# Kernel tuning notes

Measured on AMD Instinct MI355X. Metric: run time of the kernel, lower is better.

The kernel has to match this reference:

```python
import jax, jax.numpy as jnp
import numpy as np

NUM_HEADS = 16
ROPE_BASE = 10000.0


def _rotate_half(x):
    x1 = x[..., ::2]
    x2 = x[..., 1::2]
    return jnp.stack((-x2, x1), axis=-1).reshape(x.shape)


def _rope_tables(seq_len, head_dim, dtype):
    inv_freq = 1.0 / (ROPE_BASE ** (jnp.arange(0, head_dim, 2, dtype=jnp.float32) / head_dim))
    t = jnp.arange(seq_len, dtype=jnp.float32)
    freqs = jnp.outer(t, inv_freq)            # [S, head_dim//2]
    emb = jnp.concatenate((freqs, freqs), -1)  # [S, head_dim]
    return jnp.cos(emb).astype(dtype), jnp.sin(emb).astype(dtype)


def setup_inputs() -> dict:
    key = jax.random.key(0)
    ks = jax.random.split(key, 5)
    B, S, H = 1, 4096, 1024
    scale = 1.0 / np.sqrt(H)
    return {
        "x": jax.random.normal(ks[0], (B, S, H), jnp.float32),
        "Wq": jax.random.normal(ks[1], (H, H), jnp.float32) * scale,
        "Wk": jax.random.normal(ks[2], (H, H), jnp.float32) * scale,
        "Wv": jax.random.normal(ks[3], (H, H), jnp.float32) * scale,
        "Wo": jax.random.normal(ks[4], (H, H), jnp.float32) * scale,
        "attention_mask": jnp.ones((B, S), jnp.int32),
    }


def reference(x, Wq, Wk, Wv, Wo, attention_mask):
    B, S, H = x.shape
    hd = H // NUM_HEADS

    def split_heads(t):  # [B,S,H] -> [B,nh,S,hd]
        return t.reshape(B, S, NUM_HEADS, hd).transpose(0, 2, 1, 3)

    q = split_heads(x @ Wq)
    k = split_heads(x @ Wk)
    v = split_heads(x @ Wv)

    cos, sin = _rope_tables(S, hd, x.dtype)
    cos = cos[None, None]  # [1,1,S,hd]
    sin = sin[None, None]
    q = q * cos + _rotate_half(q) * sin
    k = k * cos + _rotate_half(k) * sin

    scores = jnp.einsum("bhqd,bhkd->bhqk", q, k) / jnp.sqrt(jnp.asarray(hd, x.dtype))
    mask = attention_mask.reshape(B, 1, 1, S)
    scores = jnp.where(mask == 0, jnp.finfo(x.dtype).min, scores)
    probs = jax.nn.softmax(scores, axis=-1)
    ctx = jnp.einsum("bhqk,bhkd->bhqd", probs, v)
    ctx = ctx.transpose(0, 2, 1, 3).reshape(B, S, H)
    return ctx @ Wo
```

## Files before the change

kernel.cpp:

```cpp
#include <hip/hip_runtime.h>
#include <cstdint>
#include <cstddef>

#define S_LEN 4096
#define NHEADS 16
#define HD 64
#define HDIM 1024

typedef _Float16 f16x8 __attribute__((ext_vector_type(8)));
typedef __fp16 h16x2 __attribute__((ext_vector_type(2)));
typedef float f32x4 __attribute__((ext_vector_type(4)));
typedef unsigned char uchar;
typedef unsigned int u32;

__device__ __forceinline__ f32x4 mfma16h(f16x8 a, f16x8 b, f32x4 c) {
    return __builtin_amdgcn_mfma_f32_16x16x32_f16(a, b, c, 0, 0, 0);
}
__device__ __forceinline__ void async16(void* lds, const void* g) {
    __builtin_amdgcn_global_load_lds(
        (const __attribute__((address_space(1))) u32*)g,
        (__attribute__((address_space(3))) u32*)lds, 16, 0, 0);
}


__global__ __launch_bounds__(256) void pack_xw(
    const float* __restrict__ X, uchar* __restrict__ P,
    const int* __restrict__ M, _Float16* __restrict__ FM16,
    const float* __restrict__ W0, const float* __restrict__ W1,
    const float* __restrict__ W2, const float* __restrict__ W3,
    uchar* __restrict__ PW)
{
    if (blockIdx.x < 2048) {
        int id = blockIdx.x * 256 + threadIdx.x;
        int m = id >> 7, g = id & 127;
        int kc = g >> 3, b = g & 7;
        float v[8];
        *(float4*)&v[0] = *(const float4*)&X[(size_t)m * HDIM + kc * 64 + b * 8];
        *(float4*)&v[4] = *(const float4*)&X[(size_t)m * HDIM + kc * 64 + b * 8 + 4];
        __align__(16) _Float16 h[8];
        #pragma unroll
        for (int i = 0; i < 8; i++) h[i] = (_Float16)v[i];
        size_t base = ((size_t)(m * 16 + kc)) * 128 + (size_t)((b ^ (m & 7)) * 16);
        *(uint4*)(P + base) = *(const uint4*)h;
        if (id < S_LEN) {
            int c = id >> 7, k128 = id & 127;
            int w = k128 >> 5, k32 = k128 & 31;
            int q = (k32 >> 2) & 3, kt = k32 >> 4, r = k32 & 3;
            FM16[c * 128 + w * 32 + q * 8 + kt * 4 + r] =
                (_Float16)((M[id] == 0) ? 0.0f : 1.0f);
        }
    } else {
        int id = (blockIdx.x - 2048) * 256 + threadIdx.x;
        int wsel = id >> 17;
        int lid  = id & 131071;
        int g = lid >> 10, n = lid & 1023;
        int kc = g >> 3, b = g & 7;
        const float* W = (wsel == 0) ? W0 : (wsel == 1) ? W1 : (wsel == 2) ? W2 : W3;
        uchar* dst = PW + (size_t)wsel * 2097152;
        float v[8];
        #pragma unroll
        for (int j = 0; j < 8; j++)
            v[j] = W[(size_t)(kc * 64 + b * 8 + j) * HDIM + n];
        __align__(16) _Float16 h[8];
        #pragma unroll
        for (int i = 0; i < 8; i++) h[i] = (_Float16)v[i];
        size_t base = ((size_t)(n * 16 + kc)) * 128 + (size_t)((b ^ (n & 7)) * 16);
        *(uint4*)(dst + base) = *(const uint4*)h;
    }
}

__global__ __launch_bounds__(256) void gemm_qkv(
    const uchar* __restrict__ Ap, const uchar* __restrict__ Bp,
    const int* __restrict__ M,
    uchar* __restrict__ Qg, uchar* __restrict__ Kg, uchar* __restrict__ Vg)
{
    __shared__ __align__(16) uchar AB[65536];
    const int t = threadIdx.x, lane = t & 63, w = t >> 6;
    const int quad = lane >> 4, l15 = lane & 15, x7 = l15 & 7;
    const int m0 = blockIdx.y * 128, n0 = blockIdx.x * 128;
    const int wm = (w >> 1) * 64, wn = (w & 1) * 64;

    f32x4 acc[4][4];
    const f32x4 zero4 = {0.0f, 0.0f, 0.0f, 0.0f};
    #pragma unroll
    for (int mt = 0; mt < 4; mt++)
        #pragma unroll
        for (int nt = 0; nt < 4; nt++) acc[mt][nt] = zero4;

    #pragma unroll
    for (int i = 0; i < 4; i++) {
        int idx = i * 256 + t;
        int row = idx >> 3, blk = idx & 7;
        int ldso = (idx & ~63) * 16;
        async16(AB + ldso,         Ap + ((size_t)((m0 + row) * 16 + 0)) * 128 + blk * 16);
        async16(AB + 16384 + ldso, Bp + ((size_t)((n0 + row) * 16 + 0)) * 128 + blk * 16);
    }

    for (int kc = 0; kc < 16; kc++) {
        uchar* As = AB + (kc & 1) * 32768;
        uchar* Bs = As + 16384;
        __syncthreads();
        if (kc + 1 < 16) {
            uchar* An = AB + ((kc + 1) & 1) * 32768;
            #pragma unroll
            for (int i = 0; i < 4; i++) {
                int idx = i * 256 + t;
                int row = idx >> 3, blk = idx & 7;
                int ldso = (idx & ~63) * 16;
                async16(An + ldso,
                        Ap + ((size_t)((m0 + row) * 16 + kc + 1)) * 128 + blk * 16);
                async16(An + 16384 + ldso,
                        Bp + ((size_t)((n0 + row) * 16 + kc + 1)) * 128 + blk * 16);
            }
        }
        #pragma unroll
        for (int ks = 0; ks < 2; ks++) {
            const int phys = ((ks * 4 + quad) ^ x7) * 16;
            f16x8 ah[4];
            #pragma unroll
            for (int mt = 0; mt < 4; mt++)
                ah[mt] = *(const f16x8*)(As + (size_t)(wm + mt * 16 + l15) * 128 + phys);
            #pragma unroll
            for (int nt = 0; nt < 4; nt++) {
                f16x8 bh = *(const f16x8*)(Bs + (size_t)(wn + nt * 16 + l15) * 128 + phys);
                #pragma unroll
                for (int mt = 0; mt < 4; mt++)
                    acc[mt][nt] = mfma16h(ah[mt], bh, acc[mt][nt]);
            }
        }
    }

    const int headN = (n0 + wn) >> 6;
    if (headN < 32) {
        const bool isQ = headN < 16;
        uchar* dst = isQ ? Qg : Kg;
        const int hh = headN & 15;
        const float scale = isQ ? 0.18033688011112042f : 1.0f;
        const float L32 = 13.287712379549449f / 32.0f;
        #pragma unroll
        for (int nt = 0; nt < 4; nt++) {
            const int d = nt * 16 + l15;
            const float f = __builtin_amdgcn_exp2f(-(float)(d & 31) * L32);
            const float sgn = (d & 1) ? 1.0f : -1.0f;
            #pragma unroll
            for (int mt = 0; mt < 4; mt++)
                #pragma unroll
                for (int r = 0; r < 4; r++) {
                    int m = m0 + wm + mt * 16 + quad * 4 + r;
                    float own = acc[mt][nt][r];
                    float par = __shfl_xor(own, 1);
                    float th = (float)m * f;
                    float val = (own * __cosf(th) + sgn * par * __sinf(th)) * scale;
                    _Float16 hv = (_Float16)val;
                    size_t base = ((size_t)(hh * S_LEN + m)) * 128 +
                                  (size_t)(((d >> 3) ^ (m & 7)) * 16) + (d & 7) * 2;
                    *(_Float16*)(dst + base) = hv;
                }
        }
    } else {
        const int head = headN - 32;
        const int kc2 = m0 >> 7;
        #pragma unroll
        for (int mt = 0; mt < 4; mt++) {
            int mb = m0 + wm + mt * 16 + quad * 4;
            int4 mk = *(const int4*)&M[mb];
            int wv = (wm + mt * 16) >> 5;
            int kt = mt & 1;
            int slotbase = wv * 32 + quad * 8 + kt * 4;
            #pragma unroll
            for (int nt = 0; nt < 4; nt++) {
                const int d = nt * 16 + l15;
                __align__(8) _Float16 hv[4];
                hv[0] = (mk.x == 0) ? (_Float16)0.0f : (_Float16)acc[mt][nt][0];
                hv[1] = (mk.y == 0) ? (_Float16)0.0f : (_Float16)acc[mt][nt][1];
                hv[2] = (mk.z == 0) ? (_Float16)0.0f : (_Float16)acc[mt][nt][2];
                hv[3] = (mk.w == 0) ? (_Float16)0.0f : (_Float16)acc[mt][nt][3];
                size_t row = ((size_t)(head * 32 + kc2)) * 16384 + (size_t)d * 256;
                size_t boff = (size_t)((((slotbase >> 3) ^ (d & 7)) * 16) +
                                       (slotbase & 7) * 2);
                *(ushort4*)(Vg + row + boff) = *(const ushort4*)hv;
            }
        }
    }
}

__global__ __launch_bounds__(256) void gemm_f16(
    const uchar* __restrict__ Ap, const uchar* __restrict__ Bp,
    float* __restrict__ C)
{
    __shared__ __align__(16) uchar AB[65536];
    const int t = threadIdx.x, lane = t & 63, w = t >> 6;
    const int quad = lane >> 4, l15 = lane & 15, x7 = l15 & 7;
    const int m0 = blockIdx.y * 128, n0 = blockIdx.x * 128;
    const int wm = (w >> 1) * 64, wn = (w & 1) * 64;

    f32x4 acc[4][4];
    const f32x4 zero4 = {0.0f, 0.0f, 0.0f, 0.0f};
    #pragma unroll
    for (int mt = 0; mt < 4; mt++)
        #pragma unroll
        for (int nt = 0; nt < 4; nt++) acc[mt][nt] = zero4;

    #pragma unroll
    for (int i = 0; i < 4; i++) {
        int idx = i * 256 + t;
        int row = idx >> 3, blk = idx & 7;
        int ldso = (idx & ~63) * 16;
        async16(AB + ldso,         Ap + ((size_t)((m0 + row) * 16 + 0)) * 128 + blk * 16);
        async16(AB + 16384 + ldso, Bp + ((size_t)((n0 + row) * 16 + 0)) * 128 + blk * 16);
    }

    for (int kc = 0; kc < 16; kc++) {
        uchar* As = AB + (kc & 1) * 32768;
        uchar* Bs = As + 16384;
        __syncthreads();
        if (kc + 1 < 16) {
            uchar* An = AB + ((kc + 1) & 1) * 32768;
            #pragma unroll
            for (int i = 0; i < 4; i++) {
                int idx = i * 256 + t;
                int row = idx >> 3, blk = idx & 7;
                int ldso = (idx & ~63) * 16;
                async16(An + ldso,
                        Ap + ((size_t)((m0 + row) * 16 + kc + 1)) * 128 + blk * 16);
                async16(An + 16384 + ldso,
                        Bp + ((size_t)((n0 + row) * 16 + kc + 1)) * 128 + blk * 16);
            }
        }
        #pragma unroll
        for (int ks = 0; ks < 2; ks++) {
            const int phys = ((ks * 4 + quad) ^ x7) * 16;
            f16x8 ah[4];
            #pragma unroll
            for (int mt = 0; mt < 4; mt++)
                ah[mt] = *(const f16x8*)(As + (size_t)(wm + mt * 16 + l15) * 128 + phys);
            #pragma unroll
            for (int nt = 0; nt < 4; nt++) {
                f16x8 bh = *(const f16x8*)(Bs + (size_t)(wn + nt * 16 + l15) * 128 + phys);
                #pragma unroll
                for (int mt = 0; mt < 4; mt++)
                    acc[mt][nt] = mfma16h(ah[mt], bh, acc[mt][nt]);
            }
        }
    }

    #pragma unroll
    for (int mt = 0; mt < 4; mt++)
        #pragma unroll
        for (int nt = 0; nt < 4; nt++)
            #pragma unroll
            for (int r = 0; r < 4; r++) {
                int m = m0 + wm + mt * 16 + quad * 4 + r;
                int n = n0 + wn + nt * 16 + l15;
                C[(size_t)m * HDIM + n] = acc[mt][nt][r];
            }
}

#define ISSUE_K(CC)                                                            \
  {                                                                            \
    const uchar* ks_ = kgb + (size_t)(CC) * 16384;                             \
    async16(KB,        ks_ + l16);                                             \
    async16(KB + 1024, ks_ + 1024 + l16);                                      \
    async16(KB + 2048, ks_ + 2048 + l16);                                      \
    async16(KB + 3072, ks_ + 3072 + l16);                                      \
  }
#define ISSUE_V(CC)                                                            \
  {                                                                            \
    const uchar* vs_ = vgb + (size_t)(CC) * 16384;                             \
    async16(VB,        vs_ + voff);                                            \
    async16(VB + 1024, vs_ + 4096 + voff);                                     \
    async16(VB + 2048, vs_ + 8192 + voff);                                     \
    async16(VB + 3072, vs_ + 12288 + voff);                                    \
  }

#define ATTN_STEP(CC, TOPC, MIDC, FLG)                                         \
  {                                                                            \
    asm volatile("s_waitcnt vmcnt(" TOPC ")" ::: "memory");                    \
    const int ph0_ = (quad ^ x7) * 16;                                         \
    const int ph1_ = ((4 + quad) ^ x7) * 16;                                   \
    f16x8 ka_ = *(const f16x8*)(KB + (size_t)l15 * 128 + ph0_);                \
    f16x8 kb_ = *(const f16x8*)(KB + (size_t)(16 + l15) * 128 + ph0_);         \
    f16x8 kc_ = *(const f16x8*)(KB + (size_t)l15 * 128 + ph1_);                \
    f16x8 kd_ = *(const f16x8*)(KB + (size_t)(16 + l15) * 128 + ph1_);         \
    asm volatile("s_waitcnt lgkmcnt(0)" ::: "memory");                         \
    if ((CC) + 1 < 32) ISSUE_K((CC) + 1);                                      \
    f16x8 pb[4];                                                               \
    _Pragma("unroll")                                                          \
    for (int qt = 0; qt < 4; qt++) {                                           \
      f32x4 s0 = mfma16h(ka_, qf[qt][0], zero4);                               \
      s0 = mfma16h(kc_, qf[qt][1], s0);                                        \
      f32x4 s1 = mfma16h(kb_, qf[qt][0], zero4);                               \
      s1 = mfma16h(kd_, qf[qt][1], s1);                                        \
      h16x2 c01 = __builtin_amdgcn_cvt_pkrtz(                                  \
          __builtin_amdgcn_exp2f(s0[0]), __builtin_amdgcn_exp2f(s0[1]));       \
      h16x2 c23 = __builtin_amdgcn_cvt_pkrtz(                                  \
          __builtin_amdgcn_exp2f(s0[2]), __builtin_amdgcn_exp2f(s0[3]));       \
      h16x2 c45 = __builtin_amdgcn_cvt_pkrtz(                                  \
          __builtin_amdgcn_exp2f(s1[0]), __builtin_amdgcn_exp2f(s1[1]));       \
      h16x2 c67 = __builtin_amdgcn_cvt_pkrtz(                                  \
          __builtin_amdgcn_exp2f(s1[2]), __builtin_amdgcn_exp2f(s1[3]));       \
      uint4 pw;                                                                \
      pw.x = __builtin_bit_cast(u32, c01);                                     \
      pw.y = __builtin_bit_cast(u32, c23);                                     \
      pw.z = __builtin_bit_cast(u32, c45);                                     \
      pw.w = __builtin_bit_cast(u32, c67);                                     \
      pb[qt] = __builtin_bit_cast(f16x8, pw);                                  \
    }                                                                          \
    asm volatile("s_waitcnt vmcnt(" MIDC ")" ::: "memory");                    \
    _Pragma("unroll")                                                          \
    for (int dt = 0; dt < 4; dt++) {                                           \
      f16x8 va = *(const f16x8*)(VB + (size_t)(dt * 16 + l15) * 64 + vrd);     \
      _Pragma("unroll")                                                        \
      for (int qt = 0; qt < 4; qt++)                                           \
        o[dt][qt] = mfma16h(va, pb[qt], o[dt][qt]);                            \
    }                                                                          \
    _Pragma("unroll")                                                          \
    for (int qt = 0; qt < 4; qt++)                                             \
      lacc[qt] = mfma16h((FLG), pb[qt], lacc[qt]);                             \
    asm volatile("s_waitcnt lgkmcnt(0)" ::: "memory");                         \
    if ((CC) + 1 < 32) ISSUE_V((CC) + 1);                                      \
    if ((CC) + 2 < 32) (FLG) = *(const f16x8*)(fmw + (size_t)((CC) + 2) * 256);\
  }

__global__ __launch_bounds__(256, 2) void attn9(
    const uchar* __restrict__ Qg, const uchar* __restrict__ Kg,
    const uchar* __restrict__ Vg, const uchar* __restrict__ fm16,
    uchar* __restrict__ CTXp)
{
    __shared__ __align__(16) uchar arena[32768];
    __shared__ float Lsh[4][64];
    __shared__ float Lfin[64];
    float* Os = (float*)arena;

    const int t    = threadIdx.x;
    const int lane = t & 63;
    const int w    = t >> 6;
    const int quad = lane >> 4;
    const int l15  = lane & 15;
    const int x7   = l15 & 7;

    const int flat = (int)blockIdx.x + ((int)blockIdx.y << 6);
    const int nf   = ((flat & 7) << 7) + (flat >> 3);
    const int hh   = nf >> 6;
    const int m0   = (nf & 63) * 64;

    const uchar* qgb = Qg + (size_t)hh * (S_LEN * 128);
    const uchar* kgb = Kg + (size_t)hh * (S_LEN * 128) + (size_t)w * 4096;
    const uchar* vgb = Vg + (size_t)hh * 32 * 16384;
    const uchar* fmw = fm16 + w * 64 + quad * 16;

    uchar* WB = arena + w * 8192;
    uchar* KB = WB;
    uchar* VB = WB + 4096;

    const int l16 = lane * 16;
    const int vphys = ((w * 4 + ((lane & 3) ^ ((lane >> 2) & 3))) ^ ((lane >> 2) & 7));
    const int voff  = (lane >> 2) * 256 + vphys * 16;
    const int vrd   = (quad ^ (l15 & 3)) * 16;

    f16x8 qf[4][2];
    #pragma unroll
    for (int qt = 0; qt < 4; qt++)
        #pragma unroll
        for (int ks = 0; ks < 2; ks++)
            qf[qt][ks] = *(const f16x8*)(qgb + (size_t)(m0 + qt * 16 + l15) * 128 +
                                         (size_t)(((ks * 4 + quad) ^ x7) * 16));

    f32x4 o[4][4], lacc[4];
    const f32x4 zero4 = {0.0f, 0.0f, 0.0f, 0.0f};
    #pragma unroll
    for (int dt = 0; dt < 4; dt++)
        #pragma unroll
        for (int qt = 0; qt < 4; qt++) o[dt][qt] = zero4;
    #pragma unroll
    for (int qt = 0; qt < 4; qt++) lacc[qt] = zero4;

    f16x8 flagA = *(const f16x8*)(fmw);
    f16x8 flagB = *(const f16x8*)(fmw + 256);
    asm volatile("" ::: "memory");
    ISSUE_K(0);
    ISSUE_V(0);

    ATTN_STEP(0, "4", "4", flagA);
    ATTN_STEP(1, "5", "4", flagB);
    for (int c = 2; c < 30; c += 2) {
        ATTN_STEP(c,     "5", "4", flagA);
        ATTN_STEP(c + 1, "5", "4", flagB);
    }
    ATTN_STEP(30, "5", "4", flagA);
    ATTN_STEP(31, "4", "0", flagB);

    __syncthreads();
    if (quad == 0) {
        #pragma unroll
        for (int qt = 0; qt < 4; qt++)
            Lsh[w][qt * 16 + l15] = lacc[qt][0];
    }
    __syncthreads();
    if (t < 64)
        Lfin[t] = Lsh[0][t] + Lsh[1][t] + Lsh[2][t] + Lsh[3][t];
    __syncthreads();

    for (int wv = 0; wv < 4; wv++) {
        if (w == wv) {
            #pragma unroll
            for (int dt = 0; dt < 4; dt++)
                #pragma unroll
                for (int qt = 0; qt < 4; qt++)
                    #pragma unroll
                    for (int r = 0; r < 4; r++) {
                        int q = qt * 16 + l15;
                        int d = dt * 16 + quad * 4 + r;
                        float val = o[dt][qt][r];
                        if (wv == 0) Os[q * 68 + d] = val;
                        else         Os[q * 68 + d] += val;
                    }
        }
        __syncthreads();
    }

    #pragma unroll
    for (int i = 0; i < 4; i++) {
        int idx = t + 256 * i;
        int q   = idx >> 4;
        int c4  = (idx & 15) * 4;
        float inv = 1.0f / Lfin[q];
        float4 v = *(const float4*)&Os[q * 68 + c4];
        int m = m0 + q;
        __align__(8) _Float16 h[4];
        h[0] = (_Float16)(v.x * inv);
        h[1] = (_Float16)(v.y * inv);
        h[2] = (_Float16)(v.z * inv);
        h[3] = (_Float16)(v.w * inv);
        size_t base = ((size_t)(m * 16 + hh)) * 128 +
                      (size_t)((((c4 >> 3) ^ (m & 7))) * 16) + (c4 & 7) * 2;
        *(ushort4*)(CTXp + base) = *(const ushort4*)h;
    }
}

extern "C" void kernel_launch(void* const* d_in, const int* in_sizes, int n_in,
                              void* d_out, int out_size, void* d_ws, size_t ws_size,
                              hipStream_t stream)
{
    const float* x   = (const float*)d_in[0];
    const float* Wq  = (const float*)d_in[1];
    const float* Wk  = (const float*)d_in[2];
    const float* Wv  = (const float*)d_in[3];
    const float* Wo  = (const float*)d_in[4];
    const int* amask = (const int*)d_in[5];
    float* out = (float*)d_out;

    uchar* Xp   = (uchar*)d_ws;
    uchar* Wt4  = (uchar*)d_ws + 8388608;
    uchar* Qg   = (uchar*)d_ws + 16777216;
    uchar* Kg   = (uchar*)d_ws + 25165824;
    uchar* Vg   = (uchar*)d_ws + 33554432;
    _Float16* Fm16 = (_Float16*)((uchar*)d_ws + 41943040);
    uchar* CTXp = Xp;

    dim3 blk(256);

    pack_xw<<<4096, blk, 0, stream>>>(x, Xp, amask, Fm16, Wq, Wk, Wv, Wo, Wt4);

    gemm_qkv<<<dim3(24, 32), blk, 0, stream>>>(Xp, Wt4, amask, Qg, Kg, Vg);

    attn9<<<dim3(S_LEN / 64, NHEADS), blk, 0, stream>>>(Qg, Kg, Vg,
                                                        (const uchar*)Fm16, CTXp);

    gemm_f16<<<dim3(8, 32), blk, 0, stream>>>(CTXp, Wt4 + 6291456, out);
}
```

Before: 219.8 us.

## Double-buffer V tiles in attention loop and parallelize cross-wave output reduction

V staging in LDS is now double-buffered per wave, so the next V chunk is issued together with the next K chunk right after the K reads. Before, the next V load could only start after the current PV MFMAs had finished reading the buffer, so issuing earlier gives each V load more time to arrive. The vmcnt wait counts are adjusted to match. The epilogue replaces the serialized four-wave accumulation into one LDS buffer, which needed four barriers, with two partial buffers written in two phases and summed during the final store. LDS per block grows from 32 KB to 48 KB, which may reduce occupancy at two blocks per CU.

```diff
diff --git a/kernel.cpp b/kernel.cpp
--- a/kernel.cpp
+++ b/kernel.cpp
@@ -266,11 +266,12 @@
   }
 #define ISSUE_V(CC)                                                            \
   {                                                                            \
+    uchar* vb_ = VB0 + (size_t)((CC) & 1) * 4096;                              \
     const uchar* vs_ = vgb + (size_t)(CC) * 16384;                             \
-    async16(VB,        vs_ + voff);                                            \
-    async16(VB + 1024, vs_ + 4096 + voff);                                     \
-    async16(VB + 2048, vs_ + 8192 + voff);                                     \
-    async16(VB + 3072, vs_ + 12288 + voff);                                    \
+    async16(vb_,        vs_ + voff);                                           \
+    async16(vb_ + 1024, vs_ + 4096 + voff);                                    \
+    async16(vb_ + 2048, vs_ + 8192 + voff);                                    \
+    async16(vb_ + 3072, vs_ + 12288 + voff);                                   \
   }
 
 #define ATTN_STEP(CC, TOPC, MIDC, FLG)                                         \
@@ -283,7 +284,10 @@
     f16x8 kc_ = *(const f16x8*)(KB + (size_t)l15 * 128 + ph1_);                \
     f16x8 kd_ = *(const f16x8*)(KB + (size_t)(16 + l15) * 128 + ph1_);         \
     asm volatile("s_waitcnt lgkmcnt(0)" ::: "memory");                         \
-    if ((CC) + 1 < 32) ISSUE_K((CC) + 1);                                      \
+    if ((CC) + 1 < 32) {                                                       \
+      ISSUE_K((CC) + 1);                                                       \
+      ISSUE_V((CC) + 1);                                                       \
+    }                                                                          \
     f16x8 pb[4];                                                               \
     _Pragma("unroll")                                                          \
     for (int qt = 0; qt < 4; qt++) {                                           \
@@ -307,18 +311,19 @@
       pb[qt] = __builtin_bit_cast(f16x8, pw);                                  \
     }                                                                          \
     asm volatile("s_waitcnt vmcnt(" MIDC ")" ::: "memory");                    \
-    _Pragma("unroll")                                                          \
-    for (int dt = 0; dt < 4; dt++) {                                           \
-      f16x8 va = *(const f16x8*)(VB + (size_t)(dt * 16 + l15) * 64 + vrd);     \
+    {                                                                          \
+      const uchar* vc_ = VB0 + (size_t)((CC) & 1) * 4096;                      \
       _Pragma("unroll")                                                        \
-      for (int qt = 0; qt < 4; qt++)                                           \
-        o[dt][qt] = mfma16h(va, pb[qt], o[dt][qt]);                            \
+      for (int dt = 0; dt < 4; dt++) {                                         \
+        f16x8 va = *(const f16x8*)(vc_ + (size_t)(dt * 16 + l15) * 64 + vrd);  \
+        _Pragma("unroll")                                                      \
+        for (int qt = 0; qt < 4; qt++)                                         \
+          o[dt][qt] = mfma16h(va, pb[qt], o[dt][qt]);                          \
+      }                                                                        \
     }                                                                          \
     _Pragma("unroll")                                                          \
     for (int qt = 0; qt < 4; qt++)                                             \
       lacc[qt] = mfma16h((FLG), pb[qt], lacc[qt]);                             \
-    asm volatile("s_waitcnt lgkmcnt(0)" ::: "memory");                         \
-    if ((CC) + 1 < 32) ISSUE_V((CC) + 1);                                      \
     if ((CC) + 2 < 32) (FLG) = *(const f16x8*)(fmw + (size_t)((CC) + 2) * 256);\
   }
 
@@ -327,10 +332,11 @@
     const uchar* __restrict__ Vg, const uchar* __restrict__ fm16,
     uchar* __restrict__ CTXp)
 {
-    __shared__ __align__(16) uchar arena[32768];
+    __shared__ __align__(16) uchar arena[49152];
     __shared__ float Lsh[4][64];
     __shared__ float Lfin[64];
-    float* Os = (float*)arena;
+    float* Os0 = (float*)arena;
+    float* Os1 = (float*)(arena + 17408);
 
     const int t    = threadIdx.x;
     const int lane = t & 63;
@@ -349,9 +355,9 @@
     const uchar* vgb = Vg + (size_t)hh * 32 * 16384;
     const uchar* fmw = fm16 + w * 64 + quad * 16;
 
-    uchar* WB = arena + w * 8192;
-    uchar* KB = WB;
-    uchar* VB = WB + 4096;
+    uchar* WB  = arena + w * 12288;
+    uchar* KB  = WB;
+    uchar* VB0 = WB + 4096;
 
     const int l16 = lane * 16;
     const int vphys = ((w * 4 + ((lane & 3) ^ ((lane >> 2) & 3))) ^ ((lane >> 2) & 7));
@@ -381,43 +387,47 @@
     ISSUE_K(0);
     ISSUE_V(0);
 
-    ATTN_STEP(0, "4", "4", flagA);
-    ATTN_STEP(1, "5", "4", flagB);
-    for (int c = 2; c < 30; c += 2) {
-        ATTN_STEP(c,     "5", "4", flagA);
-        ATTN_STEP(c + 1, "5", "4", flagB);
-    }
-    ATTN_STEP(30, "5", "4", flagA);
+    ATTN_STEP(0, "4", "8", flagA);
+    for (int c = 1; c < 29; c += 2) {
+        ATTN_STEP(c,     "5", "9", flagB);
+        ATTN_STEP(c + 1, "5", "9", flagA);
+    }
+    ATTN_STEP(29, "5", "9", flagB);
+    ATTN_STEP(30, "5", "9", flagA);
     ATTN_STEP(31, "4", "0", flagB);
 
-    __syncthreads();
     if (quad == 0) {
         #pragma unroll
         for (int qt = 0; qt < 4; qt++)
             Lsh[w][qt * 16 + l15] = lacc[qt][0];
     }
     __syncthreads();
-    if (t < 64)
-        Lfin[t] = Lsh[0][t] + Lsh[1][t] + Lsh[2][t] + Lsh[3][t];
+
+    if (w == 0 || w == 2) {
+        float* Od = (w == 0) ? Os0 : Os1;
+        #pragma unroll
+        for (int dt = 0; dt < 4; dt++)
+            #pragma unroll
+            for (int qt = 0; qt < 4; qt++)
+                #pragma unroll
+                for (int r = 0; r < 4; r++)
+                    Od[(qt * 16 + l15) * 68 + dt * 16 + quad * 4 + r] = o[dt][qt][r];
+    } else if (w == 1) {
+        Lfin[lane] = Lsh[0][lane] + Lsh[1][lane] + Lsh[2][lane] + Lsh[3][lane];
+    }
     __syncthreads();
 
-    for (int wv = 0; wv < 4; wv++) {
-        if (w == wv) {
-            #pragma unroll
-            for (int dt = 0; dt < 4; dt++)
+    if (w == 1 || w == 3) {
+        float* Od = (w == 1) ? Os0 : Os1;
+        #pragma unroll
+        for (int dt = 0; dt < 4; dt++)
+            #pragma unroll
+            for (int qt = 0; qt < 4; qt++)
                 #pragma unroll
-                for (int qt = 0; qt < 4; qt++)
-                    #pragma unroll
-                    for (int r = 0; r < 4; r++) {
-                        int q = qt * 16 + l15;
-                        int d = dt * 16 + quad * 4 + r;
-                        float val = o[dt][qt][r];
-                        if (wv == 0) Os[q * 68 + d] = val;
-                        else         Os[q * 68 + d] += val;
-                    }
-        }
-        __syncthreads();
-    }
+                for (int r = 0; r < 4; r++)
+                    Od[(qt * 16 + l15) * 68 + dt * 16 + quad * 4 + r] += o[dt][qt][r];
+    }
+    __syncthreads();
 
     #pragma unroll
     for (int i = 0; i < 4; i++) {
@@ -425,13 +435,14 @@
         int q   = idx >> 4;
         int c4  = (idx & 15) * 4;
         float inv = 1.0f / Lfin[q];
-        float4 v = *(const float4*)&Os[q * 68 + c4];
+        float4 va = *(const float4*)&Os0[q * 68 + c4];
+        float4 vb = *(const float4*)&Os1[q * 68 + c4];
         int m = m0 + q;
         __align__(8) _Float16 h[4];
-        h[0] = (_Float16)(v.x * inv);
-        h[1] = (_Float16)(v.y * inv);
-        h[2] = (_Float16)(v.z * inv);
-        h[3] = (_Float16)(v.w * inv);
+        h[0] = (_Float16)((va.x + vb.x) * inv);
+        h[1] = (_Float16)((va.y + vb.y) * inv);
+        h[2] = (_Float16)((va.z + vb.z) * inv);
+        h[3] = (_Float16)((va.w + vb.w) * inv);
         size_t base = ((size_t)(m * 16 + hh)) * 128 +
                       (size_t)((((c4 >> 3) ^ (m & 7))) * 16) + (c4 & 7) * 2;
         *(ushort4*)(CTXp + base) = *(const ushort4*)h;
```

Result: no change. 220.6 us (+0.4%).
